# Kernel tuning notes

Measured on AMD Instinct MI355X. Metric: run time of the kernel, lower is better.

The kernel has to match this reference:

```python
import jax, jax.numpy as jnp
import numpy as np

B, C, T, F = 64, 8, 2048, 128
DROP_WIDTH = 64
STRIPES_NUM = 2


def setup_inputs() -> dict:
    key = jax.random.key(0)
    k1, k2, k3 = jax.random.split(key, 3)
    input = jax.random.normal(k1, (B, C, T, F), dtype=jnp.float32)
    distances = jax.random.randint(k2, (B, STRIPES_NUM), 0, DROP_WIDTH, dtype=jnp.int32)
    bgns = jax.random.randint(k3, (B, STRIPES_NUM), 0, T - DROP_WIDTH, dtype=jnp.int32)
    return {"input": input, "distances": distances, "bgns": bgns}


def reference(input, distances, bgns):
    # input: [B, C, T, F]; stripes dropped along dim=2 (time).
    t = jnp.arange(input.shape[2], dtype=jnp.int32)  # [T]
    lo = bgns[:, :, None]                            # [B, S, 1]
    hi = (bgns + distances)[:, :, None]              # [B, S, 1]
    stripe = (t[None, None, :] >= lo) & (t[None, None, :] < hi)  # [B, S, T]
    drop = jnp.any(stripe, axis=1)                   # [B, T]
    keep = jnp.logical_not(drop)[:, None, :, None].astype(input.dtype)  # [B,1,T,1]
    return input * keep
```

## Files before the change

### kernel.cpp

```cpp
#include <hip/hip_runtime.h>


constexpr int Bn = 64;
constexpr int Cn = 8;
constexpr int Tn = 2048;
constexpr int Fn = 128;
constexpr int STRIPES = 2;

__global__ __launch_bounds__(256) void
drop_stripes_kernel(const float4* __restrict__ in,
                    const int* __restrict__ distances,
                    const int* __restrict__ bgns,
                    float4* __restrict__ out,
                    int n4)
{
    int idx = blockIdx.x * blockDim.x + threadIdx.x;
    const int stride = gridDim.x * blockDim.x;

    for (; idx < n4; idx += stride) {
        const int row = idx >> 5;
        const int t   = row & (Tn - 1);
        const int b   = row >> 14;

        const int s0 = bgns[b * STRIPES + 0];
        const int s1 = bgns[b * STRIPES + 1];
        const int d0 = distances[b * STRIPES + 0];
        const int d1 = distances[b * STRIPES + 1];

        const bool drop = ((unsigned)(t - s0) < (unsigned)d0) |
                          ((unsigned)(t - s1) < (unsigned)d1);

        if (drop) {
            out[idx] = make_float4(0.f, 0.f, 0.f, 0.f);
        } else {
            out[idx] = in[idx];
        }
    }
}

extern "C" void kernel_launch(void* const* d_in, const int* in_sizes, int n_in,
                              void* d_out, int out_size, void* d_ws, size_t ws_size,
                              hipStream_t stream)
{
    const float4* in        = (const float4*)d_in[0];
    const int*    distances = (const int*)d_in[1];
    const int*    bgns      = (const int*)d_in[2];
    float4*       out       = (float4*)d_out;

    const int n4 = out_size / 4;

    const int block = 256;
    const int grid  = 8192;

    drop_stripes_kernel<<<grid, block, 0, stream>>>(in, distances, bgns, out, n4);
}
```

Baseline: 200.0 us.

## Assign per-batch contiguous chunks per block with nontemporal unrolled loads and stores

Result: faster. 191.6 us (-4.2%).

```diff
diff --git a/kernel.cpp b/kernel.cpp
--- a/kernel.cpp
+++ b/kernel.cpp
@@ -1,5 +1,7 @@
 #include <hip/hip_runtime.h>
 
+
+typedef float f4 __attribute__((ext_vector_type(4)));
 
 constexpr int Bn = 64;
 constexpr int Cn = 8;
@@ -7,34 +9,59 @@
 constexpr int Fn = 128;
 constexpr int STRIPES = 2;
 
-__global__ __launch_bounds__(256) void
-drop_stripes_kernel(const float4* __restrict__ in,
+constexpr int N4_PER_B     = Cn * Tn * (Fn / 4);
+constexpr int BLOCKS_PER_B = 128;
+constexpr int CHUNK        = N4_PER_B / BLOCKS_PER_B;
+constexpr int BLOCK        = 256;
+constexpr int ITERS        = CHUNK / BLOCK;
+
+__global__ __launch_bounds__(BLOCK) void
+drop_stripes_kernel(const f4* __restrict__ in,
                     const int* __restrict__ distances,
                     const int* __restrict__ bgns,
-                    float4* __restrict__ out,
-                    int n4)
+                    f4* __restrict__ out)
 {
-    int idx = blockIdx.x * blockDim.x + threadIdx.x;
-    const int stride = gridDim.x * blockDim.x;
+    const int b     = blockIdx.x >> 7;
+    const int chunk = blockIdx.x & (BLOCKS_PER_B - 1);
+    const int base  = b * N4_PER_B + chunk * CHUNK;
 
-    for (; idx < n4; idx += stride) {
-        const int row = idx >> 5;
-        const int t   = row & (Tn - 1);
-        const int b   = row >> 14;
+    const int s0 = bgns[b * STRIPES + 0];
+    const int s1 = bgns[b * STRIPES + 1];
+    const int d0 = distances[b * STRIPES + 0];
+    const int d1 = distances[b * STRIPES + 1];
 
-        const int s0 = bgns[b * STRIPES + 0];
-        const int s1 = bgns[b * STRIPES + 1];
-        const int d0 = distances[b * STRIPES + 0];
-        const int d1 = distances[b * STRIPES + 1];
+    #pragma unroll
+    for (int i = 0; i < ITERS; i += 4) {
+        int idx0 = base + (i + 0) * BLOCK + threadIdx.x;
+        int idx1 = base + (i + 1) * BLOCK + threadIdx.x;
+        int idx2 = base + (i + 2) * BLOCK + threadIdx.x;
+        int idx3 = base + (i + 3) * BLOCK + threadIdx.x;
 
-        const bool drop = ((unsigned)(t - s0) < (unsigned)d0) |
-                          ((unsigned)(t - s1) < (unsigned)d1);
+        f4 v0 = __builtin_nontemporal_load(&in[idx0]);
+        f4 v1 = __builtin_nontemporal_load(&in[idx1]);
+        f4 v2 = __builtin_nontemporal_load(&in[idx2]);
+        f4 v3 = __builtin_nontemporal_load(&in[idx3]);
 
-        if (drop) {
-            out[idx] = make_float4(0.f, 0.f, 0.f, 0.f);
-        } else {
-            out[idx] = in[idx];
-        }
+        const int t0 = (idx0 >> 5) & (Tn - 1);
+        const int t1 = (idx1 >> 5) & (Tn - 1);
+        const int t2 = (idx2 >> 5) & (Tn - 1);
+        const int t3 = (idx3 >> 5) & (Tn - 1);
+
+        const bool k0 = ((unsigned)(t0 - s0) >= (unsigned)d0) & ((unsigned)(t0 - s1) >= (unsigned)d1);
+        const bool k1 = ((unsigned)(t1 - s0) >= (unsigned)d0) & ((unsigned)(t1 - s1) >= (unsigned)d1);
+        const bool k2 = ((unsigned)(t2 - s0) >= (unsigned)d0) & ((unsigned)(t2 - s1) >= (unsigned)d1);
+        const bool k3 = ((unsigned)(t3 - s0) >= (unsigned)d0) & ((unsigned)(t3 - s1) >= (unsigned)d1);
+
+        const f4 z = (f4)(0.f);
+        f4 r0 = k0 ? v0 : z;
+        f4 r1 = k1 ? v1 : z;
+        f4 r2 = k2 ? v2 : z;
+        f4 r3 = k3 ? v3 : z;
+
+        __builtin_nontemporal_store(r0, &out[idx0]);
+        __builtin_nontemporal_store(r1, &out[idx1]);
+        __builtin_nontemporal_store(r2, &out[idx2]);
+        __builtin_nontemporal_store(r3, &out[idx3]);
     }
 }
 
@@ -42,15 +69,12 @@
                               void* d_out, int out_size, void* d_ws, size_t ws_size,
                               hipStream_t stream)
 {
-    const float4* in        = (const float4*)d_in[0];
-    const int*    distances = (const int*)d_in[1];
-    const int*    bgns      = (const int*)d_in[2];
-    float4*       out       = (float4*)d_out;
+    const f4* in        = (const f4*)d_in[0];
+    const int* distances = (const int*)d_in[1];
+    const int* bgns      = (const int*)d_in[2];
+    f4* out              = (f4*)d_out;
 
-    const int n4 = out_size / 4;
+    const int grid = Bn * BLOCKS_PER_B;
 
-    const int block = 256;
-    const int grid  = 8192;
-
-    drop_stripes_kernel<<<grid, block, 0, stream>>>(in, distances, bgns, out, n4);
+    drop_stripes_kernel<<<grid, BLOCK, 0, stream>>>(in, distances, bgns, out);
 }
```
